# Optimization experiments

Hardware: AMD Instinct MI355X
Metric: run time of the kernel (lower is better)

## Reference

```python
import jax, jax.numpy as jnp
from jax import lax
import numpy as np

B, TIN, F, H, TOUT = 256, 512, 64, 512, 64


def setup_inputs() -> dict:
    key = jax.random.key(0)
    ks = jax.random.split(key, 16)
    s = 0.05

    def p(k, shape):
        return jax.random.normal(k, shape, jnp.float32) * s

    inp = {
        "x": jax.random.normal(ks[0], (B, TIN, F), jnp.float32),
        "y": jax.random.normal(ks[1], (B, TOUT), jnp.float32),
    }
    i = 2
    for name, insz in [("enc0", F), ("enc1", H), ("dec0", 1), ("dec1", H)]:
        inp[name + "_Wih"] = p(ks[i], (4 * H, insz)); i += 1
        inp[name + "_Whh"] = p(ks[i], (4 * H, H)); i += 1
        inp[name + "_bih"] = jnp.zeros((4 * H,), jnp.float32)
        inp[name + "_bhh"] = jnp.zeros((4 * H,), jnp.float32)
    inp["proj_W"] = p(ks[i], (1, H)); i += 1
    inp["proj_b"] = jnp.zeros((1,), jnp.float32)
    return inp


def _cell(xt, h, c, Wih, Whh, bih, bhh):
    # PyTorch gate order: i, f, g, o
    g = xt @ Wih.T + h @ Whh.T + bih + bhh  # [B, 4H]
    i, f, gg, o = jnp.split(g, 4, axis=-1)
    c = jax.nn.sigmoid(f) * c + jax.nn.sigmoid(i) * jnp.tanh(gg)
    h = jax.nn.sigmoid(o) * jnp.tanh(c)
    return h, c


def reference(x, y,
              enc0_Wih, enc0_Whh, enc0_bih, enc0_bhh,
              enc1_Wih, enc1_Whh, enc1_bih, enc1_bhh,
              dec0_Wih, dec0_Whh, dec0_bih, dec0_bhh,
              dec1_Wih, dec1_Whh, dec1_bih, dec1_bhh,
              proj_W, proj_b):
    Bsz = x.shape[0]
    Hd = enc0_Whh.shape[1]
    Tout = y.shape[1]
    z = jnp.zeros((Bsz, Hd), x.dtype)

    def enc_step(carry, xt):
        h0, c0, h1, c1 = carry
        h0, c0 = _cell(xt, h0, c0, enc0_Wih, enc0_Whh, enc0_bih, enc0_bhh)
        h1, c1 = _cell(h0, h1, c1, enc1_Wih, enc1_Whh, enc1_bih, enc1_bhh)
        return (h0, c0, h1, c1), None

    (h0, c0, h1, c1), _ = lax.scan(enc_step, (z, z, z, z), jnp.swapaxes(x, 0, 1))

    prev = x[:, -1, -1:]  # [B, 1]

    def dec_step(carry, _):
        h0, c0, h1, c1, prev = carry
        h0, c0 = _cell(prev, h0, c0, dec0_Wih, dec0_Whh, dec0_bih, dec0_bhh)
        h1, c1 = _cell(h0, h1, c1, dec1_Wih, dec1_Whh, dec1_bih, dec1_bhh)
        step = h1 @ proj_W.T + proj_b  # [B, 1]
        # teacher_forcing = 0.0 -> always feed model prediction back
        return (h0, c0, h1, c1, step), step[:, 0]

    _, outs = lax.scan(dec_step, (h0, c0, h1, c1, prev), None, length=Tout)
    return outs.T  # [B, Tout]
```

## Files before the change

kernel.cpp:

```cpp
#include <hip/hip_runtime.h>

#define TINN 512
#define FF 64
#define HHD 512
#define TOUTN 64

using v8h = __attribute__((ext_vector_type(8))) _Float16;
using v4h = __attribute__((ext_vector_type(4))) _Float16;
using v4f = __attribute__((ext_vector_type(4))) float;
using u32x4 = __attribute__((ext_vector_type(4))) unsigned int;
using u64 = unsigned long long;

#define AGT __HIP_MEMORY_SCOPE_AGENT

#define WOFF 0
#define GBUF_OFF 131072
#define BIAS_OFF 147712
#define WIH0_OFF 147968
#define PREV_OFF 148224
#define PART_OFF 148480
#define PROJW_OFF 149504
#define PROJB_OFF 151552
#define SMEM_TOTAL 151616

#define WS_BAR 0
#define WS_HOFF 16384
#define HBYTES (256 * HHD * 2)
#define WS_XS (WS_HOFF + 6 * HBYTES)
#define XS_TBYTES 32768
#define WS_NEED (WS_XS + (size_t)TINN * XS_TBYTES)

static __device__ __forceinline__ float sigm(float x) { return 1.0f / (1.0f + __expf(-x)); }
static __device__ __forceinline__ float tanh_f(float x) { return 1.0f - 2.0f / (1.0f + __expf(2.0f * x)); }

static __device__ __forceinline__ v8h aload16(const _Float16* p) {
  union { u64 u[2]; v8h h; } c;
  const u64* q = (const u64*)p;
  c.u[0] = __hip_atomic_load(q, __ATOMIC_RELAXED, AGT);
  c.u[1] = __hip_atomic_load(q + 1, __ATOMIC_RELAXED, AGT);
  return c.h;
}
static __device__ __forceinline__ void astore8(_Float16* p, v4h v) {
  union { u64 u; v4h h; } c;
  c.h = v;
  __hip_atomic_store((u64*)p, c.u, __ATOMIC_RELAXED, AGT);
}
static __device__ __forceinline__ void astore8z(void* p) {
  __hip_atomic_store((u64*)p, 0ull, __ATOMIC_RELAXED, AGT);
}

#if __has_builtin(__builtin_amdgcn_raw_ptr_buffer_load_b128) && \
    __has_builtin(__builtin_amdgcn_make_buffer_rsrc)
#define HAVE_BUFLOAD 1
using rsrc_t = __amdgpu_buffer_rsrc_t;
static __device__ __forceinline__ rsrc_t mkrsrc(const void* p) {
  return __builtin_amdgcn_make_buffer_rsrc((void*)p, (short)0, 0xFFFFFFFFu, 0x00020000);
}
static __device__ __forceinline__ v8h bload16(rsrc_t r, int byteOff) {
  union { u32x4 u; v8h h; } c;
  c.u = __builtin_amdgcn_raw_ptr_buffer_load_b128(r, byteOff, 0, 17);
  return c.h;
}
#endif

static __device__ __forceinline__ void signalDone(unsigned* slots, int mySlot, unsigned val) {
  __builtin_amdgcn_s_waitcnt(0);
  __syncthreads();
  if (threadIdx.x == 0)
    __hip_atomic_store(&slots[(size_t)mySlot * 16], val, __ATOMIC_RELAXED, AGT);
}

static __device__ __forceinline__ void waitFor(unsigned* slots, int t0, int t1) {
  int tid = threadIdx.x;
  if (tid < 64) {
    int tgt = (tid < 32) ? t0 : t1;
    if (tgt > 0) {
      while ((int)__hip_atomic_load(&slots[(size_t)tid * 16],
                                    __ATOMIC_RELAXED, AGT) < tgt)
        __builtin_amdgcn_s_sleep(1);
    }
  }
  __syncthreads();
#if __has_builtin(__builtin_amdgcn_sched_barrier)
  __builtin_amdgcn_sched_barrier(0);
#endif
}

static __device__ __attribute__((noinline)) void loadWeights(
    int tid, int hc0, const float* W1, int ld1, int K1,
    const float* W2, int K) {
  extern __shared__ char smem[];
  int c = tid >> 2, sub = tid & 3;
  int nt = c >> 4, l = c & 15;
  int n = nt * HHD + hc0 + l;
  int Kq = K >> 2;
  for (int k = sub * Kq; k < (sub + 1) * Kq; ++k) {
    float v;
    if (k < K1) v = W1[(size_t)n * ld1 + k];
    else        v = W2[(size_t)n * HHD + (k - K1)];
    int kc = k >> 6, ks = (k >> 5) & 1, quad = (k >> 3) & 3, j = k & 7;
    int off = (((kc * 2 + ks) * 4 + nt) * 64 + quad * 16 + l) * 16 + j * 2;
    *(_Float16*)(smem + WOFF + off) = (_Float16)v;
  }
}

template <int NC>
static __device__ __attribute__((noinline)) void gemmStep(
    int tid, int m0, int hc0, const float* xstep, const char* xsT,
    const _Float16* src1, const _Float16* src2,
    int rank1, _Float16* hout, float* creg) {
  extern __shared__ char smem[];
  int lane = tid & 63, wave = tid >> 6;
  int l15 = lane & 15, quad = lane >> 4;

  v4f zero4 = {0.f, 0.f, 0.f, 0.f};
  v4f acc0 = zero4, acc1 = zero4, acc2 = zero4, acc3 = zero4;

  int rt = (m0 >> 4) + wave;
  int hBase = rt * 16384 + lane * 16;
  const char* wb = smem + WOFF + (size_t)lane * 16;
  bool hasX = (xsT != nullptr) || (xstep != nullptr);

#if HAVE_BUFLOAD
  rsrc_t r1 = mkrsrc(src1);
  rsrc_t r2 = (src2 != nullptr) ? mkrsrc(src2) : r1;
#endif

#pragma unroll
  for (int ci = 0; ci < NC; ++ci) {
    v8h ak0, ak1;
    if (hasX && ci == 0) {
      if (xsT != nullptr) {
        const char* xb = xsT + rt * 2048 + lane * 16;
        ak0 = *(const v8h*)(xb);
        ak1 = *(const v8h*)(xb + 1024);
      } else {
        int ra = m0 + wave * 16 + l15;
        const float* xr = xstep + (size_t)ra * (TINN * FF) + quad * 8;
        v4f f00 = *(const v4f*)(xr);
        v4f f01 = *(const v4f*)(xr + 4);
        v4f f10 = *(const v4f*)(xr + 32);
        v4f f11 = *(const v4f*)(xr + 36);
#pragma unroll
        for (int e = 0; e < 4; ++e) {
          ak0[e] = (_Float16)f00[e]; ak0[4 + e] = (_Float16)f01[e];
          ak1[e] = (_Float16)f10[e]; ak1[4 + e] = (_Float16)f11[e];
        }
      }
    } else {
      int cj = hasX ? ci - 1 : ci;
      bool inS2 = (src2 != nullptr) && (cj >= 8);
      int kcL = inS2 ? cj - 8 : cj;
      int off = hBase + kcL * 2048;
#if HAVE_BUFLOAD
      ak0 = bload16(inS2 ? r2 : r1, off);
      ak1 = bload16(inS2 ? r2 : r1, off + 1024);
#else
      const _Float16* pr = (inS2 ? src2 : src1) + off / 2;
      ak0 = aload16(pr);
      ak1 = aload16(pr + 512);
#endif
    }
    const char* bb = wb + (size_t)ci * 8192;
#pragma unroll
    for (int ks = 0; ks < 2; ++ks) {
      v8h a = ks ? ak1 : ak0;
      v8h b0 = *(const v8h*)(bb + (ks * 4 + 0) * 1024);
      v8h b1 = *(const v8h*)(bb + (ks * 4 + 1) * 1024);
      v8h b2 = *(const v8h*)(bb + (ks * 4 + 2) * 1024);
      v8h b3 = *(const v8h*)(bb + (ks * 4 + 3) * 1024);
      acc0 = __builtin_amdgcn_mfma_f32_16x16x32_f16(a, b0, acc0, 0, 0, 0);
      acc1 = __builtin_amdgcn_mfma_f32_16x16x32_f16(a, b1, acc1, 0, 0, 0);
      acc2 = __builtin_amdgcn_mfma_f32_16x16x32_f16(a, b2, acc2, 0, 0, 0);
      acc3 = __builtin_amdgcn_mfma_f32_16x16x32_f16(a, b3, acc3, 0, 0, 0);
    }
  }

  float* gb = (float*)(smem + GBUF_OFF);
#pragma unroll
  for (int r = 0; r < 4; ++r) {
    int row = wave * 16 + quad * 4 + r;
    gb[row * 65 + l15] = acc0[r];
    gb[row * 65 + 16 + l15] = acc1[r];
    gb[row * 65 + 32 + l15] = acc2[r];
    gb[row * 65 + 48 + l15] = acc3[r];
  }
  __syncthreads();

  float* bias = (float*)(smem + BIAS_OFF);
  float* wih0 = (float*)(smem + WIH0_OFF);
  float* prevl = (float*)(smem + PREV_OFF);
  int m = tid >> 2, jb = (tid & 3) * 4;
  float pv = rank1 ? prevl[m] : 0.0f;
  v4h hh;
#pragma unroll
  for (int i = 0; i < 4; ++i) {
    int j = jb + i;
    float gi = gb[m * 65 + j] + bias[j];
    float gf = gb[m * 65 + 16 + j] + bias[16 + j];
    float gg = gb[m * 65 + 32 + j] + bias[32 + j];
    float go = gb[m * 65 + 48 + j] + bias[48 + j];
    if (rank1) {
      gi += pv * wih0[j]; gf += pv * wih0[16 + j];
      gg += pv * wih0[32 + j]; go += pv * wih0[48 + j];
    }
    float c = sigm(gf) * creg[i] + sigm(gi) * tanh_f(gg);
    float h = sigm(go) * tanh_f(c);
    creg[i] = c;
    hh[i] = (_Float16)h;
  }
  {
    int mg = m0 + m;
    int c0 = hc0 + jb;
    int off = (((mg >> 4) * 8 + (c0 >> 6)) * 2 + ((c0 >> 5) & 1)) * 1024 +
              ((((c0 >> 3) & 3) * 16 + (mg & 15)) * 16) + (c0 & 7) * 2;
    astore8(hout + off / 2, hh);
  }
}

__global__ void __launch_bounds__(256, 1)
seq2seq_kernel(const float* x,
               const float* e0wi, const float* e0wh, const float* e0bi, const float* e0bh,
               const float* e1wi, const float* e1wh, const float* e1bi, const float* e1bh,
               const float* d0wi, const float* d0wh, const float* d0bi, const float* d0bh,
               const float* d1wi, const float* d1wh, const float* d1bi, const float* d1bh,
               const float* pw, const float* pb,
               float* out, char* ws, int useXs) {
  extern __shared__ char smem[];
  int tid = threadIdx.x, bid = blockIdx.x;
  int group = bid >> 6;
  int r = bid & 63;
  bool isL1 = (r >= 32);
  int hcTile = r & 31;
  int hc0 = hcTile * 16;
  int m0 = group * 64;
  unsigned* slots = (unsigned*)(ws + WS_BAR) + (size_t)group * 1024;
  int mySlot = isL1 ? 32 + hcTile : hcTile;
  char* xs = useXs ? (ws + WS_XS) : nullptr;

  _Float16* h0b[4]; _Float16* h1b[2];
  h0b[0] = (_Float16*)(ws + WS_HOFF);
  h0b[1] = (_Float16*)(ws + WS_HOFF + 1 * HBYTES);
  h0b[2] = (_Float16*)(ws + WS_HOFF + 2 * HBYTES);
  h0b[3] = (_Float16*)(ws + WS_HOFF + 3 * HBYTES);
  h1b[0] = (_Float16*)(ws + WS_HOFF + 4 * HBYTES);
  h1b[1] = (_Float16*)(ws + WS_HOFF + 5 * HBYTES);

  float creg[4];
  creg[0] = 0.f; creg[1] = 0.f; creg[2] = 0.f; creg[3] = 0.f;

  {
    int t16 = r * 256 + tid;
    char* base = (t16 < 8192) ? (char*)h0b[3] : (char*)h1b[1];
    int idx = t16 & 8191;
    astore8z(base + (size_t)m0 * HHD * 2 + (size_t)idx * 8);
  }

  if (xs) {
    int m = m0 + (tid & 63);
    int cb = (tid >> 6) * 16;
    int rt = m >> 4, l15m = m & 15;
    for (int k = 0; k < 8; ++k) {
      int t = r + k * 64;
      const float* xp = x + (size_t)m * (TINN * FF) + (size_t)t * FF + cb;
      v4f f0 = *(const v4f*)(xp);
      v4f f1 = *(const v4f*)(xp + 4);
      v4f f2 = *(const v4f*)(xp + 8);
      v4f f3 = *(const v4f*)(xp + 12);
      v4h h0_, h1_, h2_, h3_;
#pragma unroll
      for (int e = 0; e < 4; ++e) {
        h0_[e] = (_Float16)f0[e]; h1_[e] = (_Float16)f1[e];
        h2_[e] = (_Float16)f2[e]; h3_[e] = (_Float16)f3[e];
      }
      char* xt = xs + (size_t)t * XS_TBYTES;
      v4h hs[4] = {h0_, h1_, h2_, h3_};
#pragma unroll
      for (int s = 0; s < 4; ++s) {
        int c0 = cb + 4 * s;
        int off = ((rt * 2 + ((c0 >> 5) & 1)) * 1024) +
                  ((((c0 >> 3) & 3) * 16 + l15m) * 16) + (c0 & 7) * 2;
        astore8((_Float16*)(xt + off), hs[s]);
      }
    }
  }

  if (!isL1) {
    loadWeights(tid, hc0, e0wi, 64, 64, e0wh, 576);
    if (tid < 64) {
      int n = (tid >> 4) * HHD + hc0 + (tid & 15);
      ((float*)(smem + BIAS_OFF))[tid] = e0bi[n] + e0bh[n];
    }
  } else {
    loadWeights(tid, hc0, e1wi, 512, 512, e1wh, 1024);
    if (tid < 64) {
      int n = (tid >> 4) * HHD + hc0 + (tid & 15);
      ((float*)(smem + BIAS_OFF))[tid] = e1bi[n] + e1bh[n];
    }
  }
  signalDone(slots, mySlot, 1);

  if (!isL1) {
    for (int p = 0; p < TINN; ++p) {
      waitFor(slots, p + 1, p - 2);
      gemmStep<9>(tid, m0, hc0, x + (size_t)p * FF,
                  xs ? xs + (size_t)p * XS_TBYTES : nullptr,
                  h0b[(p + 3) & 3], nullptr, 0, h0b[p & 3], creg);
      signalDone(slots, mySlot, p + 2);
    }
    loadWeights(tid, hc0, d0wh, 512, 512, nullptr, 512);
    if (tid < 64) {
      int n = (tid >> 4) * HHD + hc0 + (tid & 15);
      ((float*)(smem + BIAS_OFF))[tid] = d0bi[n] + d0bh[n];
      ((float*)(smem + WIH0_OFF))[tid] = d0wi[n];
    }
    for (int k = tid; k < 512; k += 256) ((float*)(smem + PROJW_OFF))[k] = pw[k];
    if (tid == 0) ((float*)(smem + PROJB_OFF))[0] = pb[0];
    for (int t = 0; t <= TOUTN; ++t) {
      int u = TINN + t;
      waitFor(slots, u + 1, u + 1);
      float* prevl = (float*)(smem + PREV_OFF);
      if (t == 0) {
        if (tid < 64)
          prevl[tid] = x[(size_t)(m0 + tid) * (TINN * FF) + 511 * 64 + 63];
      } else {
        float* part = (float*)(smem + PART_OFF);
        float* pjw = (float*)(smem + PROJW_OFF);
        const _Float16* h1base = h1b[(u + 1) & 1];
        int m = m0 + (tid >> 2);
        int rt = m >> 4, l15m = m & 15;
        int kc0 = (tid & 3) * 2;
        float s = 0.f;
#pragma unroll
        for (int kc = kc0; kc < kc0 + 2; ++kc)
#pragma unroll
          for (int ks = 0; ks < 2; ++ks)
#pragma unroll
            for (int q = 0; q < 4; ++q) {
              int off = ((rt * 8 + kc) * 2 + ks) * 1024 + ((q * 16 + l15m) * 16);
              v8h hv = aload16(h1base + off / 2);
              const float* w = pjw + kc * 64 + ks * 32 + q * 8;
#pragma unroll
              for (int e = 0; e < 8; ++e) s += (float)hv[e] * w[e];
            }
        part[tid] = s;
        __syncthreads();
        if (tid < 64) {
          float p4 = part[tid * 4] + part[tid * 4 + 1] + part[tid * 4 + 2] +
                     part[tid * 4 + 3] + ((float*)(smem + PROJB_OFF))[0];
          prevl[tid] = p4;
          if (hcTile == 0) out[(size_t)(m0 + tid) * TOUTN + (t - 1)] = p4;
        }
      }
      __syncthreads();
      if (t < TOUTN) {
        gemmStep<8>(tid, m0, hc0, nullptr, nullptr, h0b[(u + 3) & 3], nullptr,
                    1, h0b[u & 3], creg);
        signalDone(slots, mySlot, u + 2);
      }
    }
  } else {
    for (int s = 0; s < TINN; ++s) {
      waitFor(slots, s + 2, s + 1);
      gemmStep<16>(tid, m0, hc0, nullptr, nullptr, h0b[s & 3], h1b[(s + 1) & 1],
                   0, h1b[s & 1], creg);
      signalDone(slots, mySlot, s + 2);
    }
    loadWeights(tid, hc0, d1wi, 512, 512, d1wh, 1024);
    if (tid < 64) {
      int n = (tid >> 4) * HHD + hc0 + (tid & 15);
      ((float*)(smem + BIAS_OFF))[tid] = d1bi[n] + d1bh[n];
    }
    for (int t = 0; t < TOUTN; ++t) {
      int u = TINN + t;
      waitFor(slots, u + 2, u + 1);
      gemmStep<16>(tid, m0, hc0, nullptr, nullptr, h0b[u & 3], h1b[(u + 1) & 1],
                   0, h1b[u & 1], creg);
      signalDone(slots, mySlot, u + 2);
    }
  }
}

extern "C" void kernel_launch(void* const* d_in, const int* in_sizes, int n_in,
                              void* d_out, int out_size, void* d_ws, size_t ws_size,
                              hipStream_t stream) {
  const float* x = (const float*)d_in[0];
  const float* e0wi = (const float*)d_in[2];
  const float* e0wh = (const float*)d_in[3];
  const float* e0bi = (const float*)d_in[4];
  const float* e0bh = (const float*)d_in[5];
  const float* e1wi = (const float*)d_in[6];
  const float* e1wh = (const float*)d_in[7];
  const float* e1bi = (const float*)d_in[8];
  const float* e1bh = (const float*)d_in[9];
  const float* d0wi = (const float*)d_in[10];
  const float* d0wh = (const float*)d_in[11];
  const float* d0bi = (const float*)d_in[12];
  const float* d0bh = (const float*)d_in[13];
  const float* d1wi = (const float*)d_in[14];
  const float* d1wh = (const float*)d_in[15];
  const float* d1bi = (const float*)d_in[16];
  const float* d1bh = (const float*)d_in[17];
  const float* pw = (const float*)d_in[18];
  const float* pb = (const float*)d_in[19];

  int useXs = (ws_size >= WS_NEED) ? 1 : 0;
  (void)hipFuncSetAttribute((const void*)seq2seq_kernel,
                            hipFuncAttributeMaxDynamicSharedMemorySize, SMEM_TOTAL);
  (void)hipMemsetAsync(d_ws, 0, 16384, stream);
  seq2seq_kernel<<<dim3(256), dim3(256), SMEM_TOTAL, stream>>>(
      x, e0wi, e0wh, e0bi, e0bh, e1wi, e1wh, e1bi, e1bh,
      d0wi, d0wh, d0bi, d0bh, d1wi, d1wh, d1bi, d1bh,
      pw, pb, (float*)d_out, (char*)d_ws, useXs);
}
```

Baseline: 4.736 ms.

## Split role waits to overlap recurrent MFMA with cross-layer dependency wait

```diff
diff --git a/kernel.cpp b/kernel.cpp
--- a/kernel.cpp
+++ b/kernel.cpp
@@ -14,14 +14,13 @@
 #define AGT __HIP_MEMORY_SCOPE_AGENT
 
 #define WOFF 0
-#define GBUF_OFF 131072
-#define BIAS_OFF 147712
-#define WIH0_OFF 147968
-#define PREV_OFF 148224
-#define PART_OFF 148480
-#define PROJW_OFF 149504
-#define PROJB_OFF 151552
-#define SMEM_TOTAL 151616
+#define BIAS_OFF 131072
+#define WIH0_OFF 131328
+#define PREV_OFF 131584
+#define PART_OFF 131840
+#define PROJW_OFF 132864
+#define PROJB_OFF 134912
+#define SMEM_TOTAL 134976
 
 #define WS_BAR 0
 #define WS_HOFF 16384
@@ -48,6 +47,9 @@
 static __device__ __forceinline__ void astore8z(void* p) {
   __hip_atomic_store((u64*)p, 0ull, __ATOMIC_RELAXED, AGT);
 }
+static __device__ __forceinline__ void astore2(_Float16* p, float v) {
+  __hip_atomic_store(p, (_Float16)v, __ATOMIC_RELAXED, AGT);
+}
 
 #if __has_builtin(__builtin_amdgcn_raw_ptr_buffer_load_b128) && \
     __has_builtin(__builtin_amdgcn_make_buffer_rsrc)
@@ -70,20 +72,18 @@
     __hip_atomic_store(&slots[(size_t)mySlot * 16], val, __ATOMIC_RELAXED, AGT);
 }
 
-static __device__ __forceinline__ void waitFor(unsigned* slots, int t0, int t1) {
-  int tid = threadIdx.x;
-  if (tid < 64) {
-    int tgt = (tid < 32) ? t0 : t1;
-    if (tgt > 0) {
-      while ((int)__hip_atomic_load(&slots[(size_t)tid * 16],
+static __device__ __forceinline__ void waitRole(unsigned* slots, int base, int tgt) {
+  if (tgt > 0) {
+    if (threadIdx.x < 32) {
+      while ((int)__hip_atomic_load(&slots[(size_t)(base + threadIdx.x) * 16],
                                     __ATOMIC_RELAXED, AGT) < tgt)
         __builtin_amdgcn_s_sleep(1);
     }
-  }
-  __syncthreads();
+    __syncthreads();
 #if __has_builtin(__builtin_amdgcn_sched_barrier)
-  __builtin_amdgcn_sched_barrier(0);
+    __builtin_amdgcn_sched_barrier(0);
 #endif
+  }
 }
 
 static __device__ __attribute__((noinline)) void loadWeights(
@@ -104,118 +104,149 @@
   }
 }
 
-template <int NC>
-static __device__ __attribute__((noinline)) void gemmStep(
-    int tid, int m0, int hc0, const float* xstep, const char* xsT,
-    const _Float16* src1, const _Float16* src2,
-    int rank1, _Float16* hout, float* creg) {
-  extern __shared__ char smem[];
+template <int WC0>
+static __device__ __forceinline__ void mfma8(
+    const _Float16* src, int rt, int lane, const char* wbLane, v4f* acc) {
+#if HAVE_BUFLOAD
+  rsrc_t rs = mkrsrc(src);
+#endif
+#pragma unroll
+  for (int kc = 0; kc < 8; ++kc) {
+    int off = rt * 16384 + kc * 2048 + lane * 16;
+    v8h ak0, ak1;
+#if HAVE_BUFLOAD
+    ak0 = bload16(rs, off);
+    ak1 = bload16(rs, off + 1024);
+#else
+    ak0 = aload16(src + off / 2);
+    ak1 = aload16(src + (off + 1024) / 2);
+#endif
+    const char* bb = wbLane + (size_t)(WC0 + kc) * 8192;
+#pragma unroll
+    for (int ks = 0; ks < 2; ++ks) {
+      v8h a = ks ? ak1 : ak0;
+      acc[0] = __builtin_amdgcn_mfma_f32_16x16x32_f16(a, *(const v8h*)(bb + (ks * 4 + 0) * 1024), acc[0], 0, 0, 0);
+      acc[1] = __builtin_amdgcn_mfma_f32_16x16x32_f16(a, *(const v8h*)(bb + (ks * 4 + 1) * 1024), acc[1], 0, 0, 0);
+      acc[2] = __builtin_amdgcn_mfma_f32_16x16x32_f16(a, *(const v8h*)(bb + (ks * 4 + 2) * 1024), acc[2], 0, 0, 0);
+      acc[3] = __builtin_amdgcn_mfma_f32_16x16x32_f16(a, *(const v8h*)(bb + (ks * 4 + 3) * 1024), acc[3], 0, 0, 0);
+    }
+  }
+}
+
+static __device__ __forceinline__ void xChunk(
+    const char* xsT, const float* xstep, int m0, int tid,
+    const char* wbLane, v4f* acc) {
   int lane = tid & 63, wave = tid >> 6;
   int l15 = lane & 15, quad = lane >> 4;
-
-  v4f zero4 = {0.f, 0.f, 0.f, 0.f};
-  v4f acc0 = zero4, acc1 = zero4, acc2 = zero4, acc3 = zero4;
-
+  v8h ak0, ak1;
+  if (xsT != nullptr) {
+    int rt = (m0 >> 4) + wave;
+    const char* xb = xsT + rt * 2048 + lane * 16;
+    ak0 = *(const v8h*)(xb);
+    ak1 = *(const v8h*)(xb + 1024);
+  } else {
+    int ra = m0 + wave * 16 + l15;
+    const float* xr = xstep + (size_t)ra * (TINN * FF) + quad * 8;
+    v4f f00 = *(const v4f*)(xr);
+    v4f f01 = *(const v4f*)(xr + 4);
+    v4f f10 = *(const v4f*)(xr + 32);
+    v4f f11 = *(const v4f*)(xr + 36);
+#pragma unroll
+    for (int e = 0; e < 4; ++e) {
+      ak0[e] = (_Float16)f00[e]; ak0[4 + e] = (_Float16)f01[e];
+      ak1[e] = (_Float16)f10[e]; ak1[4 + e] = (_Float16)f11[e];
+    }
+  }
+#pragma unroll
+  for (int ks = 0; ks < 2; ++ks) {
+    v8h a = ks ? ak1 : ak0;
+    acc[0] = __builtin_amdgcn_mfma_f32_16x16x32_f16(a, *(const v8h*)(wbLane + (ks * 4 + 0) * 1024), acc[0], 0, 0, 0);
+    acc[1] = __builtin_amdgcn_mfma_f32_16x16x32_f16(a, *(const v8h*)(wbLane + (ks * 4 + 1) * 1024), acc[1], 0, 0, 0);
+    acc[2] = __builtin_amdgcn_mfma_f32_16x16x32_f16(a, *(const v8h*)(wbLane + (ks * 4 + 2) * 1024), acc[2], 0, 0, 0);
+    acc[3] = __builtin_amdgcn_mfma_f32_16x16x32_f16(a, *(const v8h*)(wbLane + (ks * 4 + 3) * 1024), acc[3], 0, 0, 0);
+  }
+}
+
+static __device__ __forceinline__ void epilogue(
+    int tid, int m0, int hc0, int rank1, _Float16* hout, float* creg, v4f* acc) {
+  extern __shared__ char smem[];
+  int lane = tid & 63, wave = tid >> 6;
+  int l15 = lane & 15, quad = lane >> 4;
+  float* bias = (float*)(smem + BIAS_OFF);
+  float bi = bias[l15], bf = bias[16 + l15], bg = bias[32 + l15], bo = bias[48 + l15];
+  float wi = 0.f, wf = 0.f, wg = 0.f, wo = 0.f;
+  if (rank1) {
+    float* wih0 = (float*)(smem + WIH0_OFF);
+    wi = wih0[l15]; wf = wih0[16 + l15]; wg = wih0[32 + l15]; wo = wih0[48 + l15];
+  }
+  float* prevl = (float*)(smem + PREV_OFF);
+  int c = hc0 + l15;
+  int colOff = (c >> 6) * 2048 + ((c >> 5) & 1) * 1024 + ((c >> 3) & 3) * 256 + (c & 7) * 2;
+#pragma unroll
+  for (int r = 0; r < 4; ++r) {
+    int mloc = wave * 16 + quad * 4 + r;
+    float gi = acc[0][r] + bi, gf = acc[1][r] + bf;
+    float gg = acc[2][r] + bg, go = acc[3][r] + bo;
+    if (rank1) {
+      float pv = prevl[mloc];
+      gi += pv * wi; gf += pv * wf; gg += pv * wg; go += pv * wo;
+    }
+    float cc = sigm(gf) * creg[r] + sigm(gi) * tanh_f(gg);
+    float h = sigm(go) * tanh_f(cc);
+    creg[r] = cc;
+    int m = m0 + mloc;
+    int off = (m >> 4) * 16384 + colOff + (m & 15) * 16;
+    astore2((_Float16*)((char*)hout + off), h);
+  }
+}
+
+
+static __device__ __attribute__((noinline)) void stepEnc0(
+    int tid, int m0, int hc0, unsigned* slots, int mySlot, int p,
+    const char* xsT, const float* xstep,
+    const _Float16* h0prev, _Float16* h0out, float* creg) {
+  extern __shared__ char smem[];
+  int lane = tid & 63, wave = tid >> 6;
+  v4f acc[4];
+  acc[0] = v4f{0.f, 0.f, 0.f, 0.f}; acc[1] = acc[0]; acc[2] = acc[0]; acc[3] = acc[0];
+  const char* wbLane = smem + WOFF + (size_t)lane * 16;
+  waitRole(slots, 0, p + 1);
+  xChunk(xsT, xstep, m0, tid, wbLane, acc);
+  mfma8<1>(h0prev, (m0 >> 4) + wave, lane, wbLane, acc);
+  waitRole(slots, 32, p - 2);
+  epilogue(tid, m0, hc0, 0, h0out, creg, acc);
+  signalDone(slots, mySlot, p + 2);
+}
+
+static __device__ __attribute__((noinline)) void stepL1(
+    int tid, int m0, int hc0, unsigned* slots, int mySlot, int tR1, int tR0,
+    const _Float16* h0src, const _Float16* h1prev, _Float16* h1out, float* creg) {
+  extern __shared__ char smem[];
+  int lane = tid & 63, wave = tid >> 6;
+  v4f acc[4];
+  acc[0] = v4f{0.f, 0.f, 0.f, 0.f}; acc[1] = acc[0]; acc[2] = acc[0]; acc[3] = acc[0];
+  const char* wbLane = smem + WOFF + (size_t)lane * 16;
   int rt = (m0 >> 4) + wave;
-  int hBase = rt * 16384 + lane * 16;
-  const char* wb = smem + WOFF + (size_t)lane * 16;
-  bool hasX = (xsT != nullptr) || (xstep != nullptr);
-
-#if HAVE_BUFLOAD
-  rsrc_t r1 = mkrsrc(src1);
-  rsrc_t r2 = (src2 != nullptr) ? mkrsrc(src2) : r1;
-#endif
-
-#pragma unroll
-  for (int ci = 0; ci < NC; ++ci) {
-    v8h ak0, ak1;
-    if (hasX && ci == 0) {
-      if (xsT != nullptr) {
-        const char* xb = xsT + rt * 2048 + lane * 16;
-        ak0 = *(const v8h*)(xb);
-        ak1 = *(const v8h*)(xb + 1024);
-      } else {
-        int ra = m0 + wave * 16 + l15;
-        const float* xr = xstep + (size_t)ra * (TINN * FF) + quad * 8;
-        v4f f00 = *(const v4f*)(xr);
-        v4f f01 = *(const v4f*)(xr + 4);
-        v4f f10 = *(const v4f*)(xr + 32);
-        v4f f11 = *(const v4f*)(xr + 36);
-#pragma unroll
-        for (int e = 0; e < 4; ++e) {
-          ak0[e] = (_Float16)f00[e]; ak0[4 + e] = (_Float16)f01[e];
-          ak1[e] = (_Float16)f10[e]; ak1[4 + e] = (_Float16)f11[e];
-        }
-      }
-    } else {
-      int cj = hasX ? ci - 1 : ci;
-      bool inS2 = (src2 != nullptr) && (cj >= 8);
-      int kcL = inS2 ? cj - 8 : cj;
-      int off = hBase + kcL * 2048;
-#if HAVE_BUFLOAD
-      ak0 = bload16(inS2 ? r2 : r1, off);
-      ak1 = bload16(inS2 ? r2 : r1, off + 1024);
-#else
-      const _Float16* pr = (inS2 ? src2 : src1) + off / 2;
-      ak0 = aload16(pr);
-      ak1 = aload16(pr + 512);
-#endif
-    }
-    const char* bb = wb + (size_t)ci * 8192;
-#pragma unroll
-    for (int ks = 0; ks < 2; ++ks) {
-      v8h a = ks ? ak1 : ak0;
-      v8h b0 = *(const v8h*)(bb + (ks * 4 + 0) * 1024);
-      v8h b1 = *(const v8h*)(bb + (ks * 4 + 1) * 1024);
-      v8h b2 = *(const v8h*)(bb + (ks * 4 + 2) * 1024);
-      v8h b3 = *(const v8h*)(bb + (ks * 4 + 3) * 1024);
-      acc0 = __builtin_amdgcn_mfma_f32_16x16x32_f16(a, b0, acc0, 0, 0, 0);
-      acc1 = __builtin_amdgcn_mfma_f32_16x16x32_f16(a, b1, acc1, 0, 0, 0);
-      acc2 = __builtin_amdgcn_mfma_f32_16x16x32_f16(a, b2, acc2, 0, 0, 0);
-      acc3 = __builtin_amdgcn_mfma_f32_16x16x32_f16(a, b3, acc3, 0, 0, 0);
-    }
-  }
-
-  float* gb = (float*)(smem + GBUF_OFF);
-#pragma unroll
-  for (int r = 0; r < 4; ++r) {
-    int row = wave * 16 + quad * 4 + r;
-    gb[row * 65 + l15] = acc0[r];
-    gb[row * 65 + 16 + l15] = acc1[r];
-    gb[row * 65 + 32 + l15] = acc2[r];
-    gb[row * 65 + 48 + l15] = acc3[r];
-  }
-  __syncthreads();
-
-  float* bias = (float*)(smem + BIAS_OFF);
-  float* wih0 = (float*)(smem + WIH0_OFF);
-  float* prevl = (float*)(smem + PREV_OFF);
-  int m = tid >> 2, jb = (tid & 3) * 4;
-  float pv = rank1 ? prevl[m] : 0.0f;
-  v4h hh;
-#pragma unroll
-  for (int i = 0; i < 4; ++i) {
-    int j = jb + i;
-    float gi = gb[m * 65 + j] + bias[j];
-    float gf = gb[m * 65 + 16 + j] + bias[16 + j];
-    float gg = gb[m * 65 + 32 + j] + bias[32 + j];
-    float go = gb[m * 65 + 48 + j] + bias[48 + j];
-    if (rank1) {
-      gi += pv * wih0[j]; gf += pv * wih0[16 + j];
-      gg += pv * wih0[32 + j]; go += pv * wih0[48 + j];
-    }
-    float c = sigm(gf) * creg[i] + sigm(gi) * tanh_f(gg);
-    float h = sigm(go) * tanh_f(c);
-    creg[i] = c;
-    hh[i] = (_Float16)h;
-  }
-  {
-    int mg = m0 + m;
-    int c0 = hc0 + jb;
-    int off = (((mg >> 4) * 8 + (c0 >> 6)) * 2 + ((c0 >> 5) & 1)) * 1024 +
-              ((((c0 >> 3) & 3) * 16 + (mg & 15)) * 16) + (c0 & 7) * 2;
-    astore8(hout + off / 2, hh);
-  }
+  waitRole(slots, 32, tR1);
+  mfma8<8>(h1prev, rt, lane, wbLane, acc);
+  waitRole(slots, 0, tR0);
+  mfma8<0>(h0src, rt, lane, wbLane, acc);
+  epilogue(tid, m0, hc0, 0, h1out, creg, acc);
+  signalDone(slots, mySlot, tR0);
+}
+
+static __device__ __attribute__((noinline)) void stepDec0(
+    int tid, int m0, int hc0, unsigned* slots, int mySlot, int u,
+    const _Float16* h0prev, _Float16* h0out, float* creg) {
+  extern __shared__ char smem[];
+  int lane = tid & 63, wave = tid >> 6;
+  v4f acc[4];
+  acc[0] = v4f{0.f, 0.f, 0.f, 0.f}; acc[1] = acc[0]; acc[2] = acc[0]; acc[3] = acc[0];
+  const char* wbLane = smem + WOFF + (size_t)lane * 16;
+  waitRole(slots, 0, u + 1);
+  mfma8<0>(h0prev, (m0 >> 4) + wave, lane, wbLane, acc);
+  epilogue(tid, m0, hc0, 1, h0out, creg, acc);
+  signalDone(slots, mySlot, u + 2);
 }
 
 __global__ void __launch_bounds__(256, 1)
@@ -278,8 +309,8 @@
 #pragma unroll
       for (int s = 0; s < 4; ++s) {
         int c0 = cb + 4 * s;
-        int off = ((rt * 2 + ((c0 >> 5) & 1)) * 1024) +
-                  ((((c0 >> 3) & 3) * 16 + l15m) * 16) + (c0 & 7) * 2;
+        int off = (rt * 2 + ((c0 >> 5) & 1)) * 1024 +
+                  ((c0 >> 3) & 3) * 256 + l15m * 16 + (c0 & 7) * 2;
         astore8((_Float16*)(xt + off), hs[s]);
       }
     }
@@ -301,13 +332,11 @@
   signalDone(slots, mySlot, 1);
 
   if (!isL1) {
-    for (int p = 0; p < TINN; ++p) {
-      waitFor(slots, p + 1, p - 2);
-      gemmStep<9>(tid, m0, hc0, x + (size_t)p * FF,
-                  xs ? xs + (size_t)p * XS_TBYTES : nullptr,
-                  h0b[(p + 3) & 3], nullptr, 0, h0b[p & 3], creg);
-      signalDone(slots, mySlot, p + 2);
-    }
+    for (int p = 0; p < TINN; ++p)
+      stepEnc0(tid, m0, hc0, slots, mySlot, p,
+               xs ? xs + (size_t)p * XS_TBYTES : nullptr,
+               xs ? nullptr : x + (size_t)p * FF,
+               h0b[(p + 3) & 3], h0b[p & 3], creg);
     loadWeights(tid, hc0, d0wh, 512, 512, nullptr, 512);
     if (tid < 64) {
       int n = (tid >> 4) * HHD + hc0 + (tid & 15);
@@ -318,7 +347,7 @@
     if (tid == 0) ((float*)(smem + PROJB_OFF))[0] = pb[0];
     for (int t = 0; t <= TOUTN; ++t) {
       int u = TINN + t;
-      waitFor(slots, u + 1, u + 1);
+      waitRole(slots, 32, u + 1);
       float* prevl = (float*)(smem + PREV_OFF);
       if (t == 0) {
         if (tid < 64)
@@ -337,7 +366,7 @@
           for (int ks = 0; ks < 2; ++ks)
 #pragma unroll
             for (int q = 0; q < 4; ++q) {
-              int off = ((rt * 8 + kc) * 2 + ks) * 1024 + ((q * 16 + l15m) * 16);
+              int off = (rt * 8 + kc) * 2048 + ks * 1024 + q * 256 + l15m * 16;
               v8h hv = aload16(h1base + off / 2);
               const float* w = pjw + kc * 64 + ks * 32 + q * 8;
 #pragma unroll
@@ -353,19 +382,13 @@
         }
       }
       __syncthreads();
-      if (t < TOUTN) {
-        gemmStep<8>(tid, m0, hc0, nullptr, nullptr, h0b[(u + 3) & 3], nullptr,
-                    1, h0b[u & 3], creg);
-        signalDone(slots, mySlot, u + 2);
-      }
+      if (t < TOUTN)
+        stepDec0(tid, m0, hc0, slots, mySlot, u, h0b[(u + 3) & 3], h0b[u & 3], creg);
     }
   } else {
-    for (int s = 0; s < TINN; ++s) {
-      waitFor(slots, s + 2, s + 1);
-      gemmStep<16>(tid, m0, hc0, nullptr, nullptr, h0b[s & 3], h1b[(s + 1) & 1],
-                   0, h1b[s & 1], creg);
-      signalDone(slots, mySlot, s + 2);
-    }
+    for (int s = 0; s < TINN; ++s)
+      stepL1(tid, m0, hc0, slots, mySlot, s + 1, s + 2,
+             h0b[s & 3], h1b[(s + 1) & 1], h1b[s & 1], creg);
     loadWeights(tid, hc0, d1wi, 512, 512, d1wh, 1024);
     if (tid < 64) {
       int n = (tid >> 4) * HHD + hc0 + (tid & 15);
@@ -373,10 +396,8 @@
     }
     for (int t = 0; t < TOUTN; ++t) {
       int u = TINN + t;
-      waitFor(slots, u + 2, u + 1);
-      gemmStep<16>(tid, m0, hc0, nullptr, nullptr, h0b[u & 3], h1b[(u + 1) & 1],
-                   0, h1b[u & 1], creg);
-      signalDone(slots, mySlot, u + 2);
+      stepL1(tid, m0, hc0, slots, mySlot, u + 1, u + 2,
+             h0b[u & 3], h1b[(u + 1) & 1], h1b[u & 1], creg);
     }
   }
 }
```

After: 6.315 ms. +33.3%, slower.
